# Kernel optimization log

Hardware: AMD Instinct MI355X
Metric: run time of the kernel (lower is better)

## Reference

```python
import jax, jax.numpy as jnp
import numpy as np
from jax import lax

B, S, I, H, O, L = 32, 512, 256, 1024, 256, 2


def _gru_layer(x_seq, h0, Wz1, Wz2, bz2, Wr1, Wr2, br2, Wg1, Wg2, bg2):
    # x_seq: [B,S,Din]; precompute all input projections in big GEMMs
    xz = jnp.einsum('bsi,hi->sbh', x_seq, Wz1)  # [S,B,H]
    xr = jnp.einsum('bsi,hi->sbh', x_seq, Wr1)
    xg = jnp.einsum('bsi,hi->sbh', x_seq, Wg1)

    def step(h, inp):
        xz_t, xr_t, xg_t = inp
        z = jax.nn.sigmoid(xz_t + h @ Wz2.T + bz2)
        r = jax.nn.sigmoid(xr_t + h @ Wr2.T + br2)
        g = jnp.tanh(xg_t + (h * r) @ Wg2.T + bg2)
        h_new = z * h + (1.0 - z) * g
        return h_new, h_new

    _, hs = lax.scan(step, h0, (xz, xr, xg))  # hs: [S,B,H] = h_1..h_S
    return hs


def setup_inputs() -> dict:
    key = jax.random.key(0)
    ks = jax.random.split(key, 32)
    d = {}
    d['x'] = jax.random.normal(ks[0], (B, S, I), dtype=jnp.float32)
    d['hidden_state'] = jnp.zeros((B, L, H), dtype=jnp.float32)
    ki = 1
    for i in range(L):
        din = I if i == 0 else H
        sc_in = 1.0 / np.sqrt(din)
        sc_h = 1.0 / np.sqrt(H)
        for gate in ('z', 'r', 'g'):
            d[f'{gate}1_{i}'] = jax.random.uniform(ks[ki], (H, din), jnp.float32, -sc_in, sc_in); ki += 1
            d[f'{gate}2_{i}'] = jax.random.uniform(ks[ki], (H, H), jnp.float32, -sc_h, sc_h); ki += 1
            d[f'{gate}2b_{i}'] = jax.random.uniform(ks[ki], (H,), jnp.float32, -sc_h, sc_h); ki += 1
    sc_y = 1.0 / np.sqrt(H)
    d['Y_w'] = jax.random.uniform(ks[ki], (O, H), jnp.float32, -sc_y, sc_y); ki += 1
    d['Y_b'] = jax.random.uniform(ks[ki], (O,), jnp.float32, -sc_y, sc_y)
    return d


def reference(x, hidden_state,
              z1_0, z2_0, z2b_0, r1_0, r2_0, r2b_0, g1_0, g2_0, g2b_0,
              z1_1, z2_1, z2b_1, r1_1, r2_1, r2b_1, g1_1, g2_1, g2b_1,
              Y_w, Y_b):
    params = [
        (z1_0, z2_0, z2b_0, r1_0, r2_0, r2b_0, g1_0, g2_0, g2b_0),
        (z1_1, z2_1, z2b_1, r1_1, r2_1, r2b_1, g1_1, g2_1, g2b_1),
    ]
    layer_in = x
    finals = []
    for i in range(L):
        h0 = hidden_state[:, i, :]
        hs = _gru_layer(layer_in, h0, *params[i])  # [S,B,H]
        # NOTE: original module returns hidden_per_t[i][seq_len-1], which is
        # the state AFTER seq_len-1 updates (second-to-last), not the final one.
        finals.append(hs[S - 2])
        layer_in = hs.transpose(1, 0, 2)  # [B,S,H]; dropout=0 -> identity
    out = jnp.einsum('bsh,oh->bso', layer_in, Y_w) + Y_b  # [B,S,O]
    hidden = jnp.stack(finals, axis=1)  # [B,L,H]
    return out, hidden
```

## Files before the change

### kernel.cpp

```cpp
#include <hip/hip_runtime.h>
#include <hip/hip_bf16.h>

typedef __bf16 bf16x8 __attribute__((ext_vector_type(8)));
typedef float  f32x4  __attribute__((ext_vector_type(4)));
typedef int    i32x4  __attribute__((ext_vector_type(4)));
typedef unsigned long long u64;

#define B_ 32
#define S_ 512
#define I_ 256
#define H_ 1024
#define O_ 256
#define M_ (B_*S_)
#define OUT_ELEMS ((size_t)B_*S_*O_)
#define BH_ (B_*H_)
#define FSTR 64

#define MFMA16(A,Bf,C) __builtin_amdgcn_mfma_f32_16x16x32_bf16(A,Bf,C,0,0,0)

union V4 { i32x4 i; bf16x8 b; };

#define LD8C(P, V) asm volatile( \
  "global_load_dwordx4 %0, %8, off\n\t" \
  "global_load_dwordx4 %1, %8, off offset:64\n\t" \
  "global_load_dwordx4 %2, %8, off offset:128\n\t" \
  "global_load_dwordx4 %3, %8, off offset:192\n\t" \
  "global_load_dwordx4 %4, %8, off offset:256\n\t" \
  "global_load_dwordx4 %5, %8, off offset:320\n\t" \
  "global_load_dwordx4 %6, %8, off offset:384\n\t" \
  "global_load_dwordx4 %7, %8, off offset:448" \
  : "=&v"((V)[0].i),"=&v"((V)[1].i),"=&v"((V)[2].i),"=&v"((V)[3].i), \
    "=&v"((V)[4].i),"=&v"((V)[5].i),"=&v"((V)[6].i),"=&v"((V)[7].i) \
  : "v"(P) : "memory")

#define WAITV() do { \
  asm volatile("s_waitcnt vmcnt(0)" ::: "memory"); \
  __builtin_amdgcn_sched_barrier(0); \
} while (0)

__device__ __forceinline__ void astore(__hip_bfloat16* p, u64 v) {
  __hip_atomic_store((u64*)p, v, __ATOMIC_RELAXED, __HIP_MEMORY_SCOPE_AGENT);
}
__device__ __forceinline__ unsigned int aload32(const unsigned int* p) {
  return __hip_atomic_load(p, __ATOMIC_RELAXED, __HIP_MEMORY_SCOPE_AGENT);
}
__device__ __forceinline__ void astore32(unsigned int* p, unsigned int v) {
  __hip_atomic_store(p, v, __ATOMIC_RELAXED, __HIP_MEMORY_SCOPE_AGENT);
}
__device__ __forceinline__ unsigned short f2bf(float f) {
  __hip_bfloat16 h = __float2bfloat16(f);
  unsigned short s; __builtin_memcpy(&s, &h, 2); return s;
}

__global__ void cvt_f32_bf16(const float* __restrict__ src, __hip_bfloat16* __restrict__ dst, int n) {
  for (int i = blockIdx.x*blockDim.x + threadIdx.x; i < n; i += gridDim.x*blockDim.x)
    dst[i] = __float2bfloat16(src[i]);
}

__global__ void xpose_x(const float* __restrict__ x, __hip_bfloat16* __restrict__ xb) {
  const int total = B_*S_*I_;
  for (int d = blockIdx.x*blockDim.x + threadIdx.x; d < total; d += gridDim.x*blockDim.x) {
    int i = d & (I_-1);
    int b = (d >> 8) & (B_-1);
    int s = d >> 13;
    xb[d] = __float2bfloat16(x[((size_t)b*S_ + s)*I_ + i]);
  }
}

__global__ __launch_bounds__(256) void gemm_out(
    const __hip_bfloat16* __restrict__ A,
    const __hip_bfloat16* __restrict__ W,
    float* __restrict__ dstf,
    const float* __restrict__ bias)
{
  __shared__ __hip_bfloat16 As[128][32];
  __shared__ __hip_bfloat16 Ws[64][32];
  const int tid  = threadIdx.x;
  const int wid  = tid >> 6, lane = tid & 63;
  const int m0   = blockIdx.y * 128, n0 = blockIdx.x * 64;
  const int col  = lane & 15, kl = (lane >> 4) * 8;
  const int lrow = tid >> 2, lcol = (tid & 3) * 8;
  f32x4 acc[2][4] = {};

  for (int k0 = 0; k0 < H_; k0 += 32) {
    __syncthreads();
    *(bf16x8*)&As[lrow][lcol]    = *(const bf16x8*)&A[(size_t)(m0+lrow)*H_    + k0 + lcol];
    *(bf16x8*)&As[lrow+64][lcol] = *(const bf16x8*)&A[(size_t)(m0+lrow+64)*H_ + k0 + lcol];
    *(bf16x8*)&Ws[lrow][lcol]    = *(const bf16x8*)&W[(size_t)(n0+lrow)*H_    + k0 + lcol];
    __syncthreads();
    bf16x8 a0 = *(const bf16x8*)&As[wid*32 + col][kl];
    bf16x8 a1 = *(const bf16x8*)&As[wid*32 + 16 + col][kl];
#pragma unroll
    for (int nt = 0; nt < 4; ++nt) {
      bf16x8 bw = *(const bf16x8*)&Ws[nt*16 + col][kl];
      acc[0][nt] = MFMA16(a0, bw, acc[0][nt]);
      acc[1][nt] = MFMA16(a1, bw, acc[1][nt]);
    }
  }
#pragma unroll
  for (int mt = 0; mt < 2; ++mt)
#pragma unroll
    for (int nt = 0; nt < 4; ++nt)
#pragma unroll
      for (int j = 0; j < 4; ++j) {
        int m = m0 + wid*32 + mt*16 + (lane>>4)*4 + j;
        int n = n0 + nt*16 + col;
        int s = m >> 5, b = m & 31;
        dstf[((size_t)b*S_ + s)*O_ + n] = acc[mt][nt][j] + bias[n];
      }
}

struct R2Args {
  const __hip_bfloat16 *xb;
  const __hip_bfloat16 *w1_0, *w2_0, *w1_1, *w2_1;
  const float *bz0,*br0,*bg0,*bz1,*br1,*bg1;
  const float *h0;
  __hip_bfloat16 *hs1;
  __hip_bfloat16 *hs2;
  __hip_bfloat16 *hr1;
  __hip_bfloat16 *hr2;
  float *fin;
  unsigned int *flag0, *flag1;
};

template<int LAY>
__device__ __forceinline__ void run_layer(const R2Args& a, int sub, int tid) {
  __shared__ f32x4 part[4][4][64];
  const int wid = tid >> 6, lane = tid & 63;
  const int col = lane & 15, kl = (lane >> 4) * 8;
  constexpr int K1 = LAY ? H_ : I_;
  constexpr int NX = K1 / 128;

  unsigned int* mf = LAY ? a.flag1 : a.flag0;
  __hip_bfloat16* hsO = LAY ? a.hs2 : a.hs1;
  __hip_bfloat16* hrO = LAY ? a.hr2 : a.hr1;
  const __hip_bfloat16* W2 = LAY ? a.w2_1 : a.w2_0;
  const __hip_bfloat16* W1 = LAY ? a.w1_1 : a.w1_0;

  bf16x8 wz2[8], wr2[8], wg2[8], wz1[NX], wr1[NX], wg1[NX];
  {
    const __hip_bfloat16* wp = W2 + (size_t)(sub*16+col)*H_ + wid*256 + kl;
#pragma unroll
    for (int kc = 0; kc < 8; ++kc) {
      wz2[kc] = *(const bf16x8*)(wp + kc*32);
      wr2[kc] = *(const bf16x8*)(wp + (size_t)H_*H_   + kc*32);
      wg2[kc] = *(const bf16x8*)(wp + (size_t)2*H_*H_ + kc*32);
    }
    const __hip_bfloat16* qp = W1 + (size_t)(sub*16+col)*K1 + wid*(K1/4) + kl;
#pragma unroll
    for (int c = 0; c < NX; ++c) {
      wz1[c] = *(const bf16x8*)(qp + c*32);
      wr1[c] = *(const bf16x8*)(qp + (size_t)H_*K1   + c*32);
      wg1[c] = *(const bf16x8*)(qp + (size_t)2*H_*K1 + c*32);
    }
  }

  const int b   = wid*16 + (lane & 15);
  const int hh0 = sub*16 + (lane >> 4)*4;
  float hreg[4] = {0,0,0,0}, zreg[4] = {0,0,0,0};
  f32x4 bz4 = {0,0,0,0}, br4 = {0,0,0,0}, bg4 = {0,0,0,0};
  if (wid < 2) {
    bz4 = *(const f32x4*)((LAY ? a.bz1 : a.bz0) + hh0);
    br4 = *(const f32x4*)((LAY ? a.br1 : a.br0) + hh0);
    bg4 = *(const f32x4*)((LAY ? a.bg1 : a.bg0) + hh0);
    f32x4 h4 = *(const f32x4*)(a.h0 + (size_t)b*2048 + LAY*1024 + hh0);
#pragma unroll
    for (int j = 0; j < 4; ++j) hreg[j] = h4[j];
  }
  if (tid < 128) {
    int bb = tid >> 2, hi = sub*16 + (tid & 3)*4;
    f32x4 v = *(const f32x4*)(a.h0 + (size_t)bb*2048 + LAY*1024 + hi);
    u64 pk = 0;
#pragma unroll
    for (int j = 0; j < 4; ++j) pk |= (u64)f2bf(v[j]) << (16*j);
    astore(&hsO[(size_t)bb*H_ + hi], pk);
  }
  __syncthreads();
  if (tid == 0) astore32(&mf[sub*FSTR], 1u);

  for (int t = 0; t < S_; ++t) {
    f32x4 az0 = {0,0,0,0}, az1 = {0,0,0,0};
    f32x4 ar0 = {0,0,0,0}, ar1 = {0,0,0,0};
    f32x4 ag0 = {0,0,0,0}, ag1 = {0,0,0,0};

    if (LAY == 0) {
      const __hip_bfloat16* p0 = a.xb + (size_t)t*(B_*K1) + (size_t)col*K1 + wid*(K1/4) + kl;
      const __hip_bfloat16* p1 = p0 + (size_t)16*K1;
      bf16x8 xs0[NX], xs1[NX];
#pragma unroll
      for (int c = 0; c < NX; ++c) {
        xs0[c] = *(const bf16x8*)(p0 + c*32);
        xs1[c] = *(const bf16x8*)(p1 + c*32);
      }
#pragma unroll
      for (int c = 0; c < NX; ++c) {
        az0 = MFMA16(wz1[c], xs0[c], az0);  az1 = MFMA16(wz1[c], xs1[c], az1);
        ar0 = MFMA16(wr1[c], xs0[c], ar0);  ar1 = MFMA16(wr1[c], xs1[c], ar1);
        ag0 = MFMA16(wg1[c], xs0[c], ag0);  ag1 = MFMA16(wg1[c], xs1[c], ag1);
      }
    }

    if (wid == 0) {
      unsigned int tgt = 2*t + 1;
      while (aload32(&mf[lane*FSTR]) < tgt) __builtin_amdgcn_s_sleep(2);
    } else if (LAY == 1 && wid == 1) {
      unsigned int tgt = 2*t + 3;
      while (aload32(&a.flag0[lane*FSTR]) < tgt) __builtin_amdgcn_s_sleep(2);
    }
    __syncthreads();

    {
      const __hip_bfloat16* hp0 = hsO + (size_t)t*BH_ + (size_t)col*H_ + wid*256 + kl;
      const __hip_bfloat16* hp1 = hp0 + (size_t)16*H_;
      V4 HV0[8], HV1[8];
      if (LAY == 1) {
        const __hip_bfloat16* p0 = a.hs1 + (size_t)(t+1)*BH_ + (size_t)col*H_ + wid*256 + kl;
        const __hip_bfloat16* p1 = p0 + (size_t)16*H_;
        V4 XV0[8], XV1[8];
        LD8C(p0, XV0); LD8C(p1, XV1);
        LD8C(hp0, HV0); LD8C(hp1, HV1);
        WAITV();
#pragma unroll
        for (int c = 0; c < 8; ++c) {
          az0 = MFMA16(wz1[c], XV0[c].b, az0);  az1 = MFMA16(wz1[c], XV1[c].b, az1);
          ar0 = MFMA16(wr1[c], XV0[c].b, ar0);  ar1 = MFMA16(wr1[c], XV1[c].b, ar1);
          ag0 = MFMA16(wg1[c], XV0[c].b, ag0);  ag1 = MFMA16(wg1[c], XV1[c].b, ag1);
        }
      } else {
        LD8C(hp0, HV0); LD8C(hp1, HV1);
        WAITV();
      }
#pragma unroll
      for (int kc = 0; kc < 8; ++kc) {
        az0 = MFMA16(wz2[kc], HV0[kc].b, az0);  az1 = MFMA16(wz2[kc], HV1[kc].b, az1);
        ar0 = MFMA16(wr2[kc], HV0[kc].b, ar0);  ar1 = MFMA16(wr2[kc], HV1[kc].b, ar1);
      }
    }
    part[wid][0][lane] = az0; part[wid][1][lane] = az1;
    part[wid][2][lane] = ar0; part[wid][3][lane] = ar1;
    __syncthreads();
    if (wid < 2) {
      f32x4 zs = part[0][wid][lane] + part[1][wid][lane] + part[2][wid][lane] + part[3][wid][lane];
      f32x4 rs = part[0][2+wid][lane] + part[1][2+wid][lane] + part[2][2+wid][lane] + part[3][2+wid][lane];
      u64 pk = 0;
#pragma unroll
      for (int j = 0; j < 4; ++j) {
        float z = 1.f / (1.f + __expf(-(zs[j] + bz4[j])));
        float r = 1.f / (1.f + __expf(-(rs[j] + br4[j])));
        zreg[j] = z;
        pk |= (u64)f2bf(r * hreg[j]) << (16*j);
      }
      astore(&hrO[(size_t)t*BH_ + (size_t)b*H_ + hh0], pk);
    }
    __syncthreads();
    if (tid == 0) astore32(&mf[sub*FSTR], 2*t + 2);
    if (wid == 0) {
      unsigned int tgt = 2*t + 2;
      while (aload32(&mf[lane*FSTR]) < tgt) __builtin_amdgcn_s_sleep(2);
    }
    __syncthreads();

    {
      const __hip_bfloat16* hp0 = hrO + (size_t)t*BH_ + (size_t)col*H_ + wid*256 + kl;
      const __hip_bfloat16* hp1 = hp0 + (size_t)16*H_;
      V4 RV0[8], RV1[8];
      LD8C(hp0, RV0); LD8C(hp1, RV1);
      WAITV();
#pragma unroll
      for (int kc = 0; kc < 8; ++kc) {
        ag0 = MFMA16(wg2[kc], RV0[kc].b, ag0);
        ag1 = MFMA16(wg2[kc], RV1[kc].b, ag1);
      }
    }
    part[wid][0][lane] = ag0; part[wid][1][lane] = ag1;
    __syncthreads();
    if (wid < 2) {
      f32x4 gs = part[0][wid][lane] + part[1][wid][lane] + part[2][wid][lane] + part[3][wid][lane];
      u64 pk = 0; f32x4 fv;
#pragma unroll
      for (int j = 0; j < 4; ++j) {
        float g  = tanhf(gs[j] + bg4[j]);
        float hn = zreg[j]*hreg[j] + (1.f - zreg[j])*g;
        hreg[j] = hn; fv[j] = hn;
        pk |= (u64)f2bf(hn) << (16*j);
      }
      astore(&hsO[(size_t)(t+1)*BH_ + (size_t)b*H_ + hh0], pk);
      if (t == S_-2) *(f32x4*)(a.fin + LAY*1024 + (size_t)b*2048 + hh0) = fv;
    }
    __syncthreads();
    if (tid == 0) astore32(&mf[sub*FSTR], 2*t + 3);
  }
}

__global__ __launch_bounds__(256, 1) void recur2(R2Args a) {
  const int lay = blockIdx.x >> 6, sub = blockIdx.x & 63;
  if (lay == 0) run_layer<0>(a, sub, threadIdx.x);
  else          run_layer<1>(a, sub, threadIdx.x);
}

extern "C" void kernel_launch(void* const* d_in, const int* in_sizes, int n_in,
                              void* d_out, int out_size, void* d_ws, size_t ws_size,
                              hipStream_t stream) {
  (void)in_sizes; (void)n_in; (void)out_size; (void)ws_size;
  const float* x     = (const float*)d_in[0];
  const float* hid0  = (const float*)d_in[1];
  const float* z1_0  = (const float*)d_in[2];
  const float* z2_0  = (const float*)d_in[3];
  const float* z2b_0 = (const float*)d_in[4];
  const float* r1_0  = (const float*)d_in[5];
  const float* r2_0  = (const float*)d_in[6];
  const float* r2b_0 = (const float*)d_in[7];
  const float* g1_0  = (const float*)d_in[8];
  const float* g2_0  = (const float*)d_in[9];
  const float* g2b_0 = (const float*)d_in[10];
  const float* z1_1  = (const float*)d_in[11];
  const float* z2_1  = (const float*)d_in[12];
  const float* z2b_1 = (const float*)d_in[13];
  const float* r1_1  = (const float*)d_in[14];
  const float* r2_1  = (const float*)d_in[15];
  const float* r2b_1 = (const float*)d_in[16];
  const float* g1_1  = (const float*)d_in[17];
  const float* g2_1  = (const float*)d_in[18];
  const float* g2b_1 = (const float*)d_in[19];
  const float* Yw    = (const float*)d_in[20];
  const float* Yb    = (const float*)d_in[21];
  float* out = (float*)d_out;

  char* ws = (char*)d_ws;
  size_t off = 0;
  auto alloc = [&](size_t bytes) -> void* {
    void* p = ws + off; off += (bytes + 255) & ~(size_t)255; return p;
  };
  __hip_bfloat16* hs1   = (__hip_bfloat16*)alloc((size_t)(S_+1)*BH_*2);
  __hip_bfloat16* hs2   = (__hip_bfloat16*)alloc((size_t)(S_+1)*BH_*2);
  __hip_bfloat16* hr1   = (__hip_bfloat16*)alloc((size_t)S_*BH_*2);
  __hip_bfloat16* hr2   = (__hip_bfloat16*)alloc((size_t)S_*BH_*2);
  __hip_bfloat16* xb    = (__hip_bfloat16*)alloc((size_t)M_*I_*2);
  __hip_bfloat16* w1p0  = (__hip_bfloat16*)alloc((size_t)3*H_*I_*2);
  __hip_bfloat16* w1p1  = (__hip_bfloat16*)alloc((size_t)3*H_*H_*2);
  __hip_bfloat16* w2p0  = (__hip_bfloat16*)alloc((size_t)3*H_*H_*2);
  __hip_bfloat16* w2p1  = (__hip_bfloat16*)alloc((size_t)3*H_*H_*2);
  __hip_bfloat16* ywp   = (__hip_bfloat16*)alloc((size_t)O_*H_*2);
  unsigned int*   bars  = (unsigned int*)  alloc(2*64*FSTR*4);

  hipMemsetAsync(bars, 0, 2*64*FSTR*4, stream);

  hipLaunchKernelGGL(xpose_x, dim3(2048), dim3(256), 0, stream, x, xb);
  auto CVT = [&](const float* s, __hip_bfloat16* d, int n) {
    hipLaunchKernelGGL(cvt_f32_bf16, dim3(512), dim3(256), 0, stream, s, d, n);
  };
  CVT(z1_0, w1p0,            H_*I_);
  CVT(r1_0, w1p0 + H_*I_,    H_*I_);
  CVT(g1_0, w1p0 + 2*H_*I_,  H_*I_);
  CVT(z2_0, w2p0,            H_*H_);
  CVT(r2_0, w2p0 + H_*H_,    H_*H_);
  CVT(g2_0, w2p0 + 2*H_*H_,  H_*H_);
  CVT(z1_1, w1p1,            H_*H_);
  CVT(r1_1, w1p1 + H_*H_,    H_*H_);
  CVT(g1_1, w1p1 + 2*H_*H_,  H_*H_);
  CVT(z2_1, w2p1,            H_*H_);
  CVT(r2_1, w2p1 + H_*H_,    H_*H_);
  CVT(g2_1, w2p1 + 2*H_*H_,  H_*H_);
  CVT(Yw,   ywp,             O_*H_);

  R2Args ra;
  ra.xb = xb;
  ra.w1_0 = w1p0; ra.w2_0 = w2p0; ra.w1_1 = w1p1; ra.w2_1 = w2p1;
  ra.bz0 = z2b_0; ra.br0 = r2b_0; ra.bg0 = g2b_0;
  ra.bz1 = z2b_1; ra.br1 = r2b_1; ra.bg1 = g2b_1;
  ra.h0 = hid0;
  ra.hs1 = hs1; ra.hs2 = hs2; ra.hr1 = hr1; ra.hr2 = hr2;
  ra.fin = out + OUT_ELEMS;
  ra.flag0 = bars; ra.flag1 = bars + 64*FSTR;
  hipLaunchKernelGGL(recur2, dim3(128), dim3(256), 0, stream, ra);

  hipLaunchKernelGGL(gemm_out, dim3(4, 128), dim3(256), 0, stream,
                     hs2 + BH_, ywp, out, Yb);
}
```

Measured before the change: 4.852 ms.

## Replace per-block flag barriers with per-wave producer flags in GRU recurrence

Replaces the single per-block step counter, which was published after a block-wide __syncthreads, with separate flags for the h and r*h buffers. Each producer wave publishes its own flag right after its stores drain (s_waitcnt vmcnt(0)). Polling moves to waves that have no compute in the gate phase and is merged into the existing syncs, which removes one __syncthreads plus one spin-wait round per half-step from the serial critical path. In exchange it polls twice as many flag lines and relies on per-wave store ordering for correctness across blocks.

```diff
diff --git a/kernel.cpp b/kernel.cpp
--- a/kernel.cpp
+++ b/kernel.cpp
@@ -120,7 +120,7 @@
   __hip_bfloat16 *hr1;
   __hip_bfloat16 *hr2;
   float *fin;
-  unsigned int *flag0, *flag1;
+  unsigned int *fl;
 };
 
 template<int LAY>
@@ -131,7 +131,14 @@
   constexpr int K1 = LAY ? H_ : I_;
   constexpr int NX = K1 / 128;
 
-  unsigned int* mf = LAY ? a.flag1 : a.flag0;
+  unsigned int* flL = a.fl + (size_t)LAY*(4*64*FSTR);
+  unsigned int* fhA = flL;
+  unsigned int* fhB = flL + 64*FSTR;
+  unsigned int* frA = flL + 128*FSTR;
+  unsigned int* frB = flL + 192*FSTR;
+  const unsigned int* fhA0 = a.fl;
+  const unsigned int* fhB0 = a.fl + 64*FSTR;
+
   __hip_bfloat16* hsO = LAY ? a.hs2 : a.hs1;
   __hip_bfloat16* hrO = LAY ? a.hr2 : a.hr1;
   const __hip_bfloat16* W2 = LAY ? a.w2_1 : a.w2_0;
@@ -166,17 +173,21 @@
     f32x4 h4 = *(const f32x4*)(a.h0 + (size_t)b*2048 + LAY*1024 + hh0);
 #pragma unroll
     for (int j = 0; j < 4; ++j) hreg[j] = h4[j];
-  }
-  if (tid < 128) {
-    int bb = tid >> 2, hi = sub*16 + (tid & 3)*4;
-    f32x4 v = *(const f32x4*)(a.h0 + (size_t)bb*2048 + LAY*1024 + hi);
     u64 pk = 0;
 #pragma unroll
-    for (int j = 0; j < 4; ++j) pk |= (u64)f2bf(v[j]) << (16*j);
-    astore(&hsO[(size_t)bb*H_ + hi], pk);
+    for (int j = 0; j < 4; ++j) pk |= (u64)f2bf(h4[j]) << (16*j);
+    astore(&hsO[(size_t)b*H_ + hh0], pk);
+    asm volatile("s_waitcnt vmcnt(0)" ::: "memory");
+    if (lane == 0) astore32((wid ? fhB : fhA) + sub*FSTR, 1u);
+  }
+  if (wid == 2) {
+    while (aload32(&fhA[lane*FSTR]) < 1u || aload32(&fhB[lane*FSTR]) < 1u)
+      __builtin_amdgcn_s_sleep(2);
+  } else if (LAY == 1 && wid == 3) {
+    while (aload32(&fhA0[lane*FSTR]) < 2u || aload32(&fhB0[lane*FSTR]) < 2u)
+      __builtin_amdgcn_s_sleep(2);
   }
   __syncthreads();
-  if (tid == 0) astore32(&mf[sub*FSTR], 1u);
 
   for (int t = 0; t < S_; ++t) {
     f32x4 az0 = {0,0,0,0}, az1 = {0,0,0,0};
@@ -199,15 +210,6 @@
         ag0 = MFMA16(wg1[c], xs0[c], ag0);  ag1 = MFMA16(wg1[c], xs1[c], ag1);
       }
     }
-
-    if (wid == 0) {
-      unsigned int tgt = 2*t + 1;
-      while (aload32(&mf[lane*FSTR]) < tgt) __builtin_amdgcn_s_sleep(2);
-    } else if (LAY == 1 && wid == 1) {
-      unsigned int tgt = 2*t + 3;
-      while (aload32(&a.flag0[lane*FSTR]) < tgt) __builtin_amdgcn_s_sleep(2);
-    }
-    __syncthreads();
 
     {
       const __hip_bfloat16* hp0 = hsO + (size_t)t*BH_ + (size_t)col*H_ + wid*256 + kl;
@@ -239,6 +241,7 @@
     part[wid][0][lane] = az0; part[wid][1][lane] = az1;
     part[wid][2][lane] = ar0; part[wid][3][lane] = ar1;
     __syncthreads();
+
     if (wid < 2) {
       f32x4 zs = part[0][wid][lane] + part[1][wid][lane] + part[2][wid][lane] + part[3][wid][lane];
       f32x4 rs = part[0][2+wid][lane] + part[1][2+wid][lane] + part[2][2+wid][lane] + part[3][2+wid][lane];
@@ -251,12 +254,12 @@
         pk |= (u64)f2bf(r * hreg[j]) << (16*j);
       }
       astore(&hrO[(size_t)t*BH_ + (size_t)b*H_ + hh0], pk);
-    }
-    __syncthreads();
-    if (tid == 0) astore32(&mf[sub*FSTR], 2*t + 2);
-    if (wid == 0) {
-      unsigned int tgt = 2*t + 2;
-      while (aload32(&mf[lane*FSTR]) < tgt) __builtin_amdgcn_s_sleep(2);
+      asm volatile("s_waitcnt vmcnt(0)" ::: "memory");
+      if (lane == 0) astore32((wid ? frB : frA) + sub*FSTR, (unsigned)(t + 1));
+    } else if (wid == 2) {
+      unsigned tgt = (unsigned)(t + 1);
+      while (aload32(&frA[lane*FSTR]) < tgt || aload32(&frB[lane*FSTR]) < tgt)
+        __builtin_amdgcn_s_sleep(2);
     }
     __syncthreads();
 
@@ -274,6 +277,7 @@
     }
     part[wid][0][lane] = ag0; part[wid][1][lane] = ag1;
     __syncthreads();
+
     if (wid < 2) {
       f32x4 gs = part[0][wid][lane] + part[1][wid][lane] + part[2][wid][lane] + part[3][wid][lane];
       u64 pk = 0; f32x4 fv;
@@ -286,9 +290,18 @@
       }
       astore(&hsO[(size_t)(t+1)*BH_ + (size_t)b*H_ + hh0], pk);
       if (t == S_-2) *(f32x4*)(a.fin + LAY*1024 + (size_t)b*2048 + hh0) = fv;
-    }
-    __syncthreads();
-    if (tid == 0) astore32(&mf[sub*FSTR], 2*t + 3);
+      asm volatile("s_waitcnt vmcnt(0)" ::: "memory");
+      if (lane == 0) astore32((wid ? fhB : fhA) + sub*FSTR, (unsigned)(t + 2));
+    } else if (wid == 2) {
+      unsigned tgt = (unsigned)(t + 2);
+      while (aload32(&fhA[lane*FSTR]) < tgt || aload32(&fhB[lane*FSTR]) < tgt)
+        __builtin_amdgcn_s_sleep(2);
+    } else if (LAY == 1 && wid == 3 && t < S_-1) {
+      unsigned tgt = (unsigned)(t + 3);
+      while (aload32(&fhA0[lane*FSTR]) < tgt || aload32(&fhB0[lane*FSTR]) < tgt)
+        __builtin_amdgcn_s_sleep(2);
+    }
+    __syncthreads();
   }
 }
 
@@ -341,9 +354,9 @@
   __hip_bfloat16* w2p0  = (__hip_bfloat16*)alloc((size_t)3*H_*H_*2);
   __hip_bfloat16* w2p1  = (__hip_bfloat16*)alloc((size_t)3*H_*H_*2);
   __hip_bfloat16* ywp   = (__hip_bfloat16*)alloc((size_t)O_*H_*2);
-  unsigned int*   bars  = (unsigned int*)  alloc(2*64*FSTR*4);
-
-  hipMemsetAsync(bars, 0, 2*64*FSTR*4, stream);
+  unsigned int*   bars  = (unsigned int*)  alloc((size_t)2*4*64*FSTR*4);
+
+  hipMemsetAsync(bars, 0, (size_t)2*4*64*FSTR*4, stream);
 
   hipLaunchKernelGGL(xpose_x, dim3(2048), dim3(256), 0, stream, x, xb);
   auto CVT = [&](const float* s, __hip_bfloat16* d, int n) {
@@ -371,7 +384,7 @@
   ra.h0 = hid0;
   ra.hs1 = hs1; ra.hs2 = hs2; ra.hr1 = hr1; ra.hr2 = hr2;
   ra.fin = out + OUT_ELEMS;
-  ra.flag0 = bars; ra.flag1 = bars + 64*FSTR;
+  ra.fl = bars;
   hipLaunchKernelGGL(recur2, dim3(128), dim3(256), 0, stream, ra);
 
   hipLaunchKernelGGL(gemm_out, dim3(4, 128), dim3(256), 0, stream,
```

New measurement: 5.703 ms. +17.5%, slower.
